# Kernel optimization log

Hardware: AMD Instinct MI355X
Metric: run time of the kernel (lower is better)

The kernel has to match this reference:

```python
import jax, jax.numpy as jnp
import numpy as np

# FP4 e2m1 lookup: nibble -> value (bit3 = sign, bits2:0 = e2m1 magnitude)
FP4_LUT = jnp.array([0.0, 0.5, 1.0, 1.5, 2.0, 3.0, 4.0, 6.0,
                     -0.0, -0.5, -1.0, -1.5, -2.0, -3.0, -4.0, -6.0], dtype=jnp.float32)
BLOCK = 16  # elements per micro-scale (one uint8 E8M0 scale per 16 fp4 values)


def _dequant(packed, sf):
    """packed: [R, K//2] int bytes (two fp4 nibbles each, low nibble first).
    sf: [R, K//16] E8M0 exponents (value = 2^(sf-127)). Returns [R, K] f32."""
    R, Kh = packed.shape
    K = Kh * 2
    lo = packed & 0xF
    hi = (packed >> 4) & 0xF
    nib = jnp.stack([lo, hi], axis=-1).reshape(R, K)
    vals = FP4_LUT[nib]  # [R, K]
    block_scale = jnp.exp2((sf - 127).astype(jnp.float32))  # [R, K//16]
    return (vals.reshape(R, K // BLOCK, BLOCK) * block_scale[:, :, None]).reshape(R, K)


def setup_inputs() -> dict:
    key = jax.random.key(0)
    ks = jax.random.split(key, 6)
    M, N, K = 8192, 4096, 4224  # K = in_features(4096) + select_num(128)
    A_packed = jax.random.randint(ks[0], (M, K // 2), 0, 256, dtype=jnp.int32)
    SFA = jax.random.randint(ks[1], (M, K // BLOCK), 118, 134, dtype=jnp.int32)
    B_packed = jax.random.randint(ks[2], (N, K // 2), 0, 256, dtype=jnp.int32)
    SFB = jax.random.randint(ks[3], (N, K // BLOCK), 118, 134, dtype=jnp.int32)
    scale = jax.random.uniform(ks[4], (1,), dtype=jnp.float32, minval=0.5, maxval=1.5)
    bias = jax.random.normal(ks[5], (N,), dtype=jnp.float32)
    return {"A_packed": A_packed, "SFA": SFA, "scale": scale,
            "B_packed": B_packed, "SFB": SFB, "bias": bias}


def reference(A_packed, SFA, scale, B_packed, SFB, bias):
    A = _dequant(A_packed, SFA)        # [M, K]
    B = _dequant(B_packed, SFB)        # [N, K]
    # y = scale * (A @ B^T) + bias   (self.scale == 1.0 folded into scale)
    y = scale[0] * jnp.einsum('mk,nk->mn', A, B) + bias[None, :]
    return y
```

## Files before the change

kernel.cpp:

```cpp
#include <hip/hip_runtime.h>
#include <stdint.h>

#define M_DIM 8192
#define N_DIM 4096
#define K_DIM 4224
#define BK 64

typedef float f32x16 __attribute__((ext_vector_type(16)));
typedef int   i32x8  __attribute__((ext_vector_type(8)));
typedef int   i32x4  __attribute__((ext_vector_type(4)));

#define RAW_BARRIER()  asm volatile("s_barrier" ::: "memory")
#define WAIT_VM4()     asm volatile("s_waitcnt vmcnt(4)" ::: "memory")
#define WAIT_VM0()     asm volatile("s_waitcnt vmcnt(0)" ::: "memory")

__device__ __forceinline__ uint32_t conv4(uint32_t x, uint32_t k1) {
    uint32_t n7   = x & 0x07070707u;
    uint32_t base = __builtin_amdgcn_perm(0x46444240u, 0x3E3C3800u, n7);
    uint32_t nz   = __builtin_amdgcn_perm(0x01010101u, 0x01010100u, n7);
    uint32_t sign = (x & 0x08080808u) << 4;
    return (base + nz * k1 - (nz << 6)) | sign;
}

__global__ __launch_bounds__(256) void dequant_all(
    const int* __restrict__ Ap, const int* __restrict__ SFA, uint8_t* __restrict__ Aout,
    const int* __restrict__ Bp, const int* __restrict__ SFB, uint8_t* __restrict__ Bout)
{
    const int nblkA = M_DIM * K_DIM / 16;
    int i = blockIdx.x * 256 + threadIdx.x;
    const int* p; const int* sf; uint8_t* out; int idx;
    if (i < nblkA) { p = Ap; sf = SFA; out = Aout; idx = i; }
    else           { p = Bp; sf = SFB; out = Bout; idx = i - nblkA; }

    const int4* p4 = (const int4*)p;
    int4 p0 = p4[2 * idx];
    int4 p1 = p4[2 * idx + 1];
    int s4 = (sf[idx] - 127) << 2;
    uint32_t k1 = (uint32_t)(s4 + 64);

    uint32_t o[4];
#pragma unroll
    for (int g = 0; g < 2; ++g) {
        int4 pg = g ? p1 : p0;
        uint32_t w = (uint32_t)(pg.x & 0xFF) | ((uint32_t)(pg.y & 0xFF) << 8) |
                     ((uint32_t)(pg.z & 0xFF) << 16) | ((uint32_t)pg.w << 24);
        uint32_t lr = conv4(w & 0x0F0F0F0Fu, k1);
        uint32_t hr = conv4((w >> 4) & 0x0F0F0F0Fu, k1);
        o[2 * g]     = __builtin_amdgcn_perm(hr, lr, 0x05010400u);
        o[2 * g + 1] = __builtin_amdgcn_perm(hr, lr, 0x07030602u);
    }
    *(uint4*)(out + (size_t)idx * 16) = make_uint4(o[0], o[1], o[2], o[3]);
}

__global__ __launch_bounds__(512, 2) void gemm_mx(
    const uint8_t* __restrict__ A, const uint8_t* __restrict__ B,
    const float* __restrict__ scale, const float* __restrict__ bias,
    float* __restrict__ C)
{
    __shared__ uint8_t smem[131072];

    const int tid  = threadIdx.x;
    const int lane = tid & 63;
    const int w    = tid >> 6;
    const int wm   = w >> 2;
    const int wn   = w & 3;
    const int r31  = lane & 31;
    const int h    = lane >> 5;

    const int lin = blockIdx.y * 16 + blockIdx.x;
    const int o   = (lin & 7) * 64 + (lin >> 3);
    const int bn0 = (o & 15) * 256;
    const int bm0 = (o >> 4) * 256;

    f32x16 acc[4][2];
#pragma unroll
    for (int i = 0; i < 4; ++i)
#pragma unroll
        for (int j = 0; j < 2; ++j)
            acc[i][j] = (f32x16)(0.0f);

    const int srow = lane >> 2;
    const int scol = (((lane & 3) ^ ((lane >> 3) & 3)) << 4);
    const uint8_t* Ag = A + (size_t)(bm0 + w * 32 + srow) * K_DIM + scol;
    const uint8_t* Bg = B + (size_t)(bn0 + w * 32 + srow) * K_DIM + scol;
    uint8_t* Asw = smem + w * 2048;
    uint8_t* Bsw = smem + 16384 + w * 2048;

#define STAGE(koff, boff)                                                        \
    do {                                                                         \
        const uint8_t* ag_ = Ag + (koff);                                        \
        const uint8_t* bg_ = Bg + (koff);                                        \
        __builtin_amdgcn_global_load_lds(                                        \
            (const __attribute__((address_space(1))) void*)(ag_),                \
            (__attribute__((address_space(3))) void*)(Asw + (boff)), 16, 0, 0);  \
        __builtin_amdgcn_global_load_lds(                                        \
            (const __attribute__((address_space(1))) void*)(ag_ + (size_t)16 * K_DIM), \
            (__attribute__((address_space(3))) void*)(Asw + (boff) + 1024), 16, 0, 0); \
        __builtin_amdgcn_global_load_lds(                                        \
            (const __attribute__((address_space(1))) void*)(bg_),                \
            (__attribute__((address_space(3))) void*)(Bsw + (boff)), 16, 0, 0);  \
        __builtin_amdgcn_global_load_lds(                                        \
            (const __attribute__((address_space(1))) void*)(bg_ + (size_t)16 * K_DIM), \
            (__attribute__((address_space(3))) void*)(Bsw + (boff) + 1024), 16, 0, 0); \
    } while (0)

    const int sx = (r31 >> 1) & 3;
    const uint8_t* pa_lo[4]; const uint8_t* pa_hi[4];
    const uint8_t* pb_lo[2]; const uint8_t* pb_hi[2];
#pragma unroll
    for (int mi = 0; mi < 4; ++mi) {
        const uint8_t* base = smem + (wm * 128 + mi * 32 + r31) * 64;
        pa_lo[mi] = base + (((2 * h)     ^ sx) << 4);
        pa_hi[mi] = base + (((2 * h + 1) ^ sx) << 4);
    }
#pragma unroll
    for (int ni = 0; ni < 2; ++ni) {
        const uint8_t* base = smem + 16384 + (wn * 64 + ni * 32 + r31) * 64;
        pb_lo[ni] = base + (((2 * h)     ^ sx) << 4);
        pb_hi[ni] = base + (((2 * h + 1) ^ sx) << 4);
    }

    i32x8 afX0[2], afX1[2], bfX0[2], bfX1[2], afY[2];

    auto rd = [&](const uint8_t* plo, const uint8_t* phi, int off, i32x8& dst) {
        i32x4 lo = *(const i32x4*)(plo + off);
        i32x4 hi = *(const i32x4*)(phi + off);
        dst = __builtin_shufflevector(lo, hi, 0, 1, 2, 3, 4, 5, 6, 7);
    };
    auto mm = [&](const i32x8& a, const i32x8& b, f32x16& c) {
        c = __builtin_amdgcn_mfma_scale_f32_32x32x64_f8f6f4(
                a, b, c, 1, 1, 0, 0x7F7F7F7F, 0, 0x7F7F7F7F);
    };

#define CORE(AC, BC, AN, BN, OBN)                             \
    __builtin_amdgcn_s_setprio(1);                            \
    mm(AC[0], BC[0], acc[0][0]); mm(AC[0], BC[1], acc[0][1]); \
    mm(AC[1], BC[0], acc[1][0]); mm(AC[1], BC[1], acc[1][1]); \
    __builtin_amdgcn_s_setprio(0);                            \
    rd(pa_lo[0], pa_hi[0], OBN, AN[0]);                       \
    rd(pa_lo[1], pa_hi[1], OBN, AN[1]);                       \
    rd(pb_lo[0], pb_hi[0], OBN, BN[0]);                       \
    rd(pb_lo[1], pb_hi[1], OBN, BN[1]);                       \
    __builtin_amdgcn_s_setprio(1);                            \
    mm(afY[0], BC[0], acc[2][0]); mm(afY[0], BC[1], acc[2][1]); \
    mm(afY[1], BC[0], acc[3][0]); mm(afY[1], BC[1], acc[3][1]); \
    __builtin_amdgcn_s_setprio(0);                            \
    rd(pa_lo[2], pa_hi[2], OBN, afY[0]);                      \
    rd(pa_lo[3], pa_hi[3], OBN, afY[1]);

#define BODY(T, AC, BC, AN, BN, OBN, OBS)                     \
    STAGE(((T) + 3) * BK, OBS);                               \
    CORE(AC, BC, AN, BN, OBN)                                 \
    WAIT_VM4(); RAW_BARRIER();

    STAGE(0 * BK, 0);
    STAGE(1 * BK, 32768);
    STAGE(2 * BK, 65536);
    WAIT_VM4();
    RAW_BARRIER();
    rd(pa_lo[0], pa_hi[0], 0, afX0[0]);
    rd(pa_lo[1], pa_hi[1], 0, afX0[1]);
    rd(pb_lo[0], pb_hi[0], 0, bfX0[0]);
    rd(pb_lo[1], pb_hi[1], 0, bfX0[1]);
    rd(pa_lo[2], pa_hi[2], 0, afY[0]);
    rd(pa_lo[3], pa_hi[3], 0, afY[1]);

#pragma unroll 1
    for (int g = 0; g < 15; ++g) {
        const int t = 4 * g;
        BODY(t,     afX0, bfX0, afX1, bfX1, 32768, 98304)
        BODY(t + 1, afX1, bfX1, afX0, bfX0, 65536, 0)
        BODY(t + 2, afX0, bfX0, afX1, bfX1, 98304, 32768)
        BODY(t + 3, afX1, bfX1, afX0, bfX0, 0,     65536)
    }
    BODY(60, afX0, bfX0, afX1, bfX1, 32768, 98304)
    BODY(61, afX1, bfX1, afX0, bfX0, 65536, 0)
    BODY(62, afX0, bfX0, afX1, bfX1, 98304, 32768)
    CORE(afX1, bfX1, afX0, bfX0, 0)
    WAIT_VM0(); RAW_BARRIER();
    CORE(afX0, bfX0, afX1, bfX1, 32768)
    __builtin_amdgcn_s_setprio(1);
    mm(afX1[0], bfX1[0], acc[0][0]); mm(afX1[0], bfX1[1], acc[0][1]);
    mm(afX1[1], bfX1[0], acc[1][0]); mm(afX1[1], bfX1[1], acc[1][1]);
    mm(afY[0],  bfX1[0], acc[2][0]); mm(afY[0],  bfX1[1], acc[2][1]);
    mm(afY[1],  bfX1[0], acc[3][0]); mm(afY[1],  bfX1[1], acc[3][1]);
    __builtin_amdgcn_s_setprio(0);
#undef BODY
#undef CORE
#undef STAGE

    const float sc = scale[0];
#pragma unroll
    for (int ni = 0; ni < 2; ++ni) {
        const int col = bn0 + wn * 64 + ni * 32 + r31;
        const float bv = bias[col];
#pragma unroll
        for (int mi = 0; mi < 4; ++mi) {
            const int rbase = bm0 + wm * 128 + mi * 32 + 4 * h;
#pragma unroll
            for (int reg = 0; reg < 16; ++reg) {
                const int row = rbase + (reg & 3) + 8 * (reg >> 2);
                C[(size_t)row * N_DIM + col] = sc * acc[mi][ni][reg] + bv;
            }
        }
    }
}

extern "C" void kernel_launch(void* const* d_in, const int* in_sizes, int n_in,
                              void* d_out, int out_size, void* d_ws, size_t ws_size,
                              hipStream_t stream) {
    const int*   A_packed = (const int*)d_in[0];
    const int*   SFA      = (const int*)d_in[1];
    const float* scale    = (const float*)d_in[2];
    const int*   B_packed = (const int*)d_in[3];
    const int*   SFB      = (const int*)d_in[4];
    const float* bias     = (const float*)d_in[5];
    float*       out      = (float*)d_out;

    uint8_t* Abf8 = (uint8_t*)d_ws;
    uint8_t* Bbf8 = Abf8 + (size_t)M_DIM * K_DIM;

    const int nblkA = M_DIM * K_DIM / 16;
    const int nblkB = N_DIM * K_DIM / 16;
    dequant_all<<<(nblkA + nblkB) / 256, 256, 0, stream>>>(
        A_packed, SFA, Abf8, B_packed, SFB, Bbf8);

    dim3 grid(N_DIM / 256, M_DIM / 256);
    gemm_mx<<<grid, 512, 0, stream>>>(Abf8, Bbf8, scale, bias, out);
}
```

Before: 342.4 us.

## Load B fragments directly from global into registers, bypassing LDS

B operand tiles are no longer staged through shared memory. Each wave now loads its B MFMA fragments straight from global memory into registers one k-step ahead. This halves LDS usage to 64KB and removes the B LDS writes and reads, and the vmcnt waits are adjusted to match. In exchange, each B row is fetched redundantly by the two wm wave-rows, and global load latency now sits in front of the MFMA chain, guarded only by a one-step prefetch and vmcnt(6).

```diff
diff --git a/kernel.cpp b/kernel.cpp
--- a/kernel.cpp
+++ b/kernel.cpp
@@ -11,6 +11,7 @@
 typedef int   i32x4  __attribute__((ext_vector_type(4)));
 
 #define RAW_BARRIER()  asm volatile("s_barrier" ::: "memory")
+#define WAIT_VM6()     asm volatile("s_waitcnt vmcnt(6)" ::: "memory")
 #define WAIT_VM4()     asm volatile("s_waitcnt vmcnt(4)" ::: "memory")
 #define WAIT_VM0()     asm volatile("s_waitcnt vmcnt(0)" ::: "memory")
 
@@ -57,7 +58,7 @@
     const float* __restrict__ scale, const float* __restrict__ bias,
     float* __restrict__ C)
 {
-    __shared__ uint8_t smem[131072];
+    __shared__ uint8_t smem[65536];
 
     const int tid  = threadIdx.x;
     const int lane = tid & 63;
@@ -82,42 +83,29 @@
     const int srow = lane >> 2;
     const int scol = (((lane & 3) ^ ((lane >> 3) & 3)) << 4);
     const uint8_t* Ag = A + (size_t)(bm0 + w * 32 + srow) * K_DIM + scol;
-    const uint8_t* Bg = B + (size_t)(bn0 + w * 32 + srow) * K_DIM + scol;
     uint8_t* Asw = smem + w * 2048;
-    uint8_t* Bsw = smem + 16384 + w * 2048;
 
 #define STAGE(koff, boff)                                                        \
     do {                                                                         \
         const uint8_t* ag_ = Ag + (koff);                                        \
-        const uint8_t* bg_ = Bg + (koff);                                        \
         __builtin_amdgcn_global_load_lds(                                        \
             (const __attribute__((address_space(1))) void*)(ag_),                \
             (__attribute__((address_space(3))) void*)(Asw + (boff)), 16, 0, 0);  \
         __builtin_amdgcn_global_load_lds(                                        \
             (const __attribute__((address_space(1))) void*)(ag_ + (size_t)16 * K_DIM), \
             (__attribute__((address_space(3))) void*)(Asw + (boff) + 1024), 16, 0, 0); \
-        __builtin_amdgcn_global_load_lds(                                        \
-            (const __attribute__((address_space(1))) void*)(bg_),                \
-            (__attribute__((address_space(3))) void*)(Bsw + (boff)), 16, 0, 0);  \
-        __builtin_amdgcn_global_load_lds(                                        \
-            (const __attribute__((address_space(1))) void*)(bg_ + (size_t)16 * K_DIM), \
-            (__attribute__((address_space(3))) void*)(Bsw + (boff) + 1024), 16, 0, 0); \
     } while (0)
+
+    const uint8_t* pgB0 = B + (size_t)(bn0 + wn * 64 + r31) * K_DIM + h * 32;
+    const uint8_t* pgB1 = pgB0 + (size_t)32 * K_DIM;
 
     const int sx = (r31 >> 1) & 3;
     const uint8_t* pa_lo[4]; const uint8_t* pa_hi[4];
-    const uint8_t* pb_lo[2]; const uint8_t* pb_hi[2];
 #pragma unroll
     for (int mi = 0; mi < 4; ++mi) {
         const uint8_t* base = smem + (wm * 128 + mi * 32 + r31) * 64;
         pa_lo[mi] = base + (((2 * h)     ^ sx) << 4);
         pa_hi[mi] = base + (((2 * h + 1) ^ sx) << 4);
-    }
-#pragma unroll
-    for (int ni = 0; ni < 2; ++ni) {
-        const uint8_t* base = smem + 16384 + (wn * 64 + ni * 32 + r31) * 64;
-        pb_lo[ni] = base + (((2 * h)     ^ sx) << 4);
-        pb_hi[ni] = base + (((2 * h + 1) ^ sx) << 4);
     }
 
     i32x8 afX0[2], afX1[2], bfX0[2], bfX1[2], afY[2];
@@ -132,15 +120,16 @@
                 a, b, c, 1, 1, 0, 0x7F7F7F7F, 0, 0x7F7F7F7F);
     };
 
-#define CORE(AC, BC, AN, BN, OBN)                             \
+#define CORE(AC, BC, AN, BN, OBN, TN)                         \
+    BN[0] = *(const i32x8*)(pgB0 + (TN) * 64);                \
+    BN[1] = *(const i32x8*)(pgB1 + (TN) * 64);                \
+    WAIT_VM6();                                               \
     __builtin_amdgcn_s_setprio(1);                            \
     mm(AC[0], BC[0], acc[0][0]); mm(AC[0], BC[1], acc[0][1]); \
     mm(AC[1], BC[0], acc[1][0]); mm(AC[1], BC[1], acc[1][1]); \
     __builtin_amdgcn_s_setprio(0);                            \
     rd(pa_lo[0], pa_hi[0], OBN, AN[0]);                       \
     rd(pa_lo[1], pa_hi[1], OBN, AN[1]);                       \
-    rd(pb_lo[0], pb_hi[0], OBN, BN[0]);                       \
-    rd(pb_lo[1], pb_hi[1], OBN, BN[1]);                       \
     __builtin_amdgcn_s_setprio(1);                            \
     mm(afY[0], BC[0], acc[2][0]); mm(afY[0], BC[1], acc[2][1]); \
     mm(afY[1], BC[0], acc[3][0]); mm(afY[1], BC[1], acc[3][1]); \
@@ -150,35 +139,64 @@
 
 #define BODY(T, AC, BC, AN, BN, OBN, OBS)                     \
     STAGE(((T) + 3) * BK, OBS);                               \
-    CORE(AC, BC, AN, BN, OBN)                                 \
-    WAIT_VM4(); RAW_BARRIER();
+    CORE(AC, BC, AN, BN, OBN, (T) + 1)                        \
+    RAW_BARRIER();
 
     STAGE(0 * BK, 0);
-    STAGE(1 * BK, 32768);
-    STAGE(2 * BK, 65536);
-    WAIT_VM4();
+    STAGE(1 * BK, 16384);
+    STAGE(2 * BK, 32768);
+    bfX0[0] = *(const i32x8*)(pgB0 + 0);
+    bfX0[1] = *(const i32x8*)(pgB1 + 0);
+    WAIT_VM0();
     RAW_BARRIER();
     rd(pa_lo[0], pa_hi[0], 0, afX0[0]);
     rd(pa_lo[1], pa_hi[1], 0, afX0[1]);
-    rd(pb_lo[0], pb_hi[0], 0, bfX0[0]);
-    rd(pb_lo[1], pb_hi[1], 0, bfX0[1]);
     rd(pa_lo[2], pa_hi[2], 0, afY[0]);
     rd(pa_lo[3], pa_hi[3], 0, afY[1]);
 
 #pragma unroll 1
     for (int g = 0; g < 15; ++g) {
         const int t = 4 * g;
-        BODY(t,     afX0, bfX0, afX1, bfX1, 32768, 98304)
-        BODY(t + 1, afX1, bfX1, afX0, bfX0, 65536, 0)
-        BODY(t + 2, afX0, bfX0, afX1, bfX1, 98304, 32768)
-        BODY(t + 3, afX1, bfX1, afX0, bfX0, 0,     65536)
-    }
-    BODY(60, afX0, bfX0, afX1, bfX1, 32768, 98304)
-    BODY(61, afX1, bfX1, afX0, bfX0, 65536, 0)
-    BODY(62, afX0, bfX0, afX1, bfX1, 98304, 32768)
-    CORE(afX1, bfX1, afX0, bfX0, 0)
-    WAIT_VM0(); RAW_BARRIER();
-    CORE(afX0, bfX0, afX1, bfX1, 32768)
+        BODY(t,     afX0, bfX0, afX1, bfX1, 16384, 49152)
+        BODY(t + 1, afX1, bfX1, afX0, bfX0, 32768, 0)
+        BODY(t + 2, afX0, bfX0, afX1, bfX1, 49152, 16384)
+        BODY(t + 3, afX1, bfX1, afX0, bfX0, 0,     32768)
+    }
+    BODY(60, afX0, bfX0, afX1, bfX1, 16384, 49152)
+    BODY(61, afX1, bfX1, afX0, bfX0, 32768, 0)
+    BODY(62, afX0, bfX0, afX1, bfX1, 49152, 16384)
+    bfX0[0] = *(const i32x8*)(pgB0 + 64 * 64);
+    bfX0[1] = *(const i32x8*)(pgB1 + 64 * 64);
+    WAIT_VM4();
+    __builtin_amdgcn_s_setprio(1);
+    mm(afX1[0], bfX1[0], acc[0][0]); mm(afX1[0], bfX1[1], acc[0][1]);
+    mm(afX1[1], bfX1[0], acc[1][0]); mm(afX1[1], bfX1[1], acc[1][1]);
+    __builtin_amdgcn_s_setprio(0);
+    rd(pa_lo[0], pa_hi[0], 0, afX0[0]);
+    rd(pa_lo[1], pa_hi[1], 0, afX0[1]);
+    __builtin_amdgcn_s_setprio(1);
+    mm(afY[0], bfX1[0], acc[2][0]); mm(afY[0], bfX1[1], acc[2][1]);
+    mm(afY[1], bfX1[0], acc[3][0]); mm(afY[1], bfX1[1], acc[3][1]);
+    __builtin_amdgcn_s_setprio(0);
+    rd(pa_lo[2], pa_hi[2], 0, afY[0]);
+    rd(pa_lo[3], pa_hi[3], 0, afY[1]);
+    RAW_BARRIER();
+    bfX1[0] = *(const i32x8*)(pgB0 + 65 * 64);
+    bfX1[1] = *(const i32x8*)(pgB1 + 65 * 64);
+    WAIT_VM4();
+    __builtin_amdgcn_s_setprio(1);
+    mm(afX0[0], bfX0[0], acc[0][0]); mm(afX0[0], bfX0[1], acc[0][1]);
+    mm(afX0[1], bfX0[0], acc[1][0]); mm(afX0[1], bfX0[1], acc[1][1]);
+    __builtin_amdgcn_s_setprio(0);
+    rd(pa_lo[0], pa_hi[0], 16384, afX1[0]);
+    rd(pa_lo[1], pa_hi[1], 16384, afX1[1]);
+    __builtin_amdgcn_s_setprio(1);
+    mm(afY[0], bfX0[0], acc[2][0]); mm(afY[0], bfX0[1], acc[2][1]);
+    mm(afY[1], bfX0[0], acc[3][0]); mm(afY[1], bfX0[1], acc[3][1]);
+    __builtin_amdgcn_s_setprio(0);
+    rd(pa_lo[2], pa_hi[2], 16384, afY[0]);
+    rd(pa_lo[3], pa_hi[3], 16384, afY[1]);
+    WAIT_VM0();
     __builtin_amdgcn_s_setprio(1);
     mm(afX1[0], bfX1[0], acc[0][0]); mm(afX1[0], bfX1[1], acc[0][1]);
     mm(afX1[1], bfX1[0], acc[1][0]); mm(afX1[1], bfX1[1], acc[1][1]);
```

After: 412.3 us. +20.4%, slower.
